# Optimization experiments

Hardware: AMD Instinct MI355X
Metric: run time of the kernel (lower is better)

## Reference

```python
import jax, jax.numpy as jnp
import numpy as np

B, L, D, H, DFF, V, NL = 8, 512, 1024, 16, 4096, 32000, 6
DH = D // H
EPS = 1e-5


def _layer_norm(x):
    # fresh nn.LayerNorm(d_model) each call: gamma=1, beta=0
    mu = jnp.mean(x, axis=-1, keepdims=True)
    var = jnp.var(x, axis=-1, keepdims=True)
    return (x - mu) / jnp.sqrt(var + EPS)


def _positional_encoding(seq_len, d_model, dtype):
    position = jnp.arange(seq_len, dtype=jnp.float32)[:, None]
    div_term = 1.0 / jnp.power(10000.0, jnp.arange(0, d_model, 2, dtype=jnp.float32) / d_model)
    pe = jnp.zeros((seq_len, d_model), dtype=jnp.float32)
    pe = pe.at[:, 0::2].set(jnp.sin(position * div_term))
    pe = pe.at[:, 1::2].set(jnp.cos(position * div_term))
    return pe.astype(dtype)  # [L, D]


def setup_inputs() -> dict:
    key = jax.random.key(0)
    ks = jax.random.split(key, 16)
    s = 0.02
    inp = {
        "sequence": jax.random.randint(ks[0], (B, L), 0, V),
        "segment_label": jax.random.randint(ks[1], (B, L), 0, 3),
        "tok_emb": jax.random.normal(ks[2], (V, D), jnp.float32) * s,
        "seg_emb": jax.random.normal(ks[3], (3, D), jnp.float32) * s,
        "Wq": jax.random.normal(ks[4], (NL, D, D), jnp.float32) * s,
        "bq": jnp.zeros((NL, D), jnp.float32),
        "Wk": jax.random.normal(ks[5], (NL, D, D), jnp.float32) * s,
        "bk": jnp.zeros((NL, D), jnp.float32),
        "Wv": jax.random.normal(ks[6], (NL, D, D), jnp.float32) * s,
        "bv": jnp.zeros((NL, D), jnp.float32),
        "Wo": jax.random.normal(ks[7], (NL, D, D), jnp.float32) * s,
        "bo": jnp.zeros((NL, D), jnp.float32),
        "W1": jax.random.normal(ks[8], (NL, D, DFF), jnp.float32) * s,
        "b1": jnp.zeros((NL, DFF), jnp.float32),
        "W2": jax.random.normal(ks[9], (NL, DFF, D), jnp.float32) * s,
        "b2": jnp.zeros((NL, D), jnp.float32),
    }
    return inp


def reference(sequence, segment_label, tok_emb, seg_emb, Wq, bq, Wk, bk, Wv, bv, Wo, bo, W1, b1, W2, b2):
    n_layers = Wq.shape[0]
    batch, seq_len = sequence.shape
    d_model = tok_emb.shape[1]
    n_heads = H
    dh = d_model // n_heads

    # pad mask: True where key token == 0; broadcast over heads and query positions
    pad = (sequence == 0)  # [B, Lk]
    mask = pad[:, None, None, :]  # [B, 1, 1, Lk]

    pe = _positional_encoding(seq_len, d_model, tok_emb.dtype)
    x = tok_emb[sequence] + pe[None, :, :] + seg_emb[segment_label]  # [B, L, D]

    for i in range(n_layers):
        residual = x
        # NOTE: original code uses a raw reshape [B, L, H*dh] -> [B, H, L, dh]
        # (no transpose); we replicate that exact math.
        q = (x @ Wq[i] + bq[i]).reshape(batch, n_heads, seq_len, dh)
        k = (x @ Wk[i] + bk[i]).reshape(batch, n_heads, seq_len, dh)
        v = (x @ Wv[i] + bv[i]).reshape(batch, n_heads, seq_len, dh)
        scores = jnp.einsum("bhqd,bhkd->bhqk", q, k) / jnp.sqrt(jnp.asarray(dh, x.dtype))
        scores = jnp.where(mask, jnp.asarray(-1e9, x.dtype), scores)
        attn = jax.nn.softmax(scores, axis=-1)
        context = jnp.einsum("bhqk,bhkd->bhqd", attn, v).reshape(batch, seq_len, n_heads * dh)
        out = context @ Wo[i] + bo[i]
        x = _layer_norm(out + residual)

        residual = x
        h = jax.nn.gelu(x @ W1[i] + b1[i], approximate=False)
        out = h @ W2[i] + b2[i]
        x = _layer_norm(residual + out)

    return x
```

## Files before the change

kernel.cpp:

```cpp
#include <hip/hip_runtime.h>
#include <cstdint>
#include <cstddef>

typedef unsigned short u16;
typedef __attribute__((ext_vector_type(8))) short short8;
typedef __attribute__((ext_vector_type(4))) float f32x4;

#define DEV __device__ __forceinline__

DEV float bf2f(u16 u) {
    union { float f; uint32_t i; } c; c.i = ((uint32_t)u) << 16; return c.f;
}
DEV u16 f2bf(float f) {
    union { float f; uint32_t i; } c; c.f = f;
    uint32_t r = c.i + 0x7FFF + ((c.i >> 16) & 1);
    return (u16)(r >> 16);
}

DEV void gload16(const void* g, void* l) {
    __builtin_amdgcn_global_load_lds(
        (const __attribute__((address_space(1))) void*)g,
        (__attribute__((address_space(3))) void*)l, 16, 0, 0);
}

template<int N> DEV void waitv() {
    if constexpr (N == 0)      asm volatile("s_waitcnt vmcnt(0)" ::: "memory");
    else if constexpr (N == 2) asm volatile("s_waitcnt vmcnt(2)" ::: "memory");
    else if constexpr (N == 3) asm volatile("s_waitcnt vmcnt(3)" ::: "memory");
    else if constexpr (N == 4) asm volatile("s_waitcnt vmcnt(4)" ::: "memory");
    else if constexpr (N == 6) asm volatile("s_waitcnt vmcnt(6)" ::: "memory");
    else if constexpr (N == 8) asm volatile("s_waitcnt vmcnt(8)" ::: "memory");
    else                       asm volatile("s_waitcnt vmcnt(0)" ::: "memory");
}

__global__ __launch_bounds__(512)
void attn_kernel(const u16* __restrict__ Qb, const u16* __restrict__ Kb,
                 const u16* __restrict__ vt, const int* __restrict__ seq,
                 u16* __restrict__ ctx)
{
    __shared__ __align__(16) u16 Ss[64 * 512];
    const int tid = threadIdx.x, lane = tid & 63, wid = tid >> 6;
    const int bh = blockIdx.y;
    const int b  = bh >> 4;
    const int q0 = blockIdx.x << 6;
    const u16* Qh = Qb + ((long)bh << 15) + (long)q0 * 64;
    const u16* Kh = Kb + ((long)bh << 15);
    const u16* Vh = vt + ((long)bh << 15);
    const int lr = lane & 15, lk = lane >> 4;

    f32x4 sacc[4][4] = {};
    {
        short8 af[4], bf[4];
#pragma unroll
        for (int s = 0; s < 2; ++s) {
#pragma unroll
            for (int m = 0; m < 4; ++m)
                af[m] = *(const short8*)(Qh + (long)(m * 16 + lr) * 64 + s * 32 + lk * 8);
#pragma unroll
            for (int n = 0; n < 4; ++n)
                bf[n] = *(const short8*)(Kh + (long)(wid * 64 + n * 16 + lr) * 64 + s * 32 + lk * 8);
#pragma unroll
            for (int m = 0; m < 4; ++m)
#pragma unroll
                for (int n = 0; n < 4; ++n)
                    sacc[m][n] = __builtin_amdgcn_mfma_f32_16x16x32_bf16(af[m], bf[n], sacc[m][n], 0, 0, 0);
        }
    }
#pragma unroll
    for (int m = 0; m < 4; ++m) {
#pragma unroll
        for (int n = 0; n < 4; ++n) {
            const int k = wid * 64 + n * 16 + lr;
#pragma unroll
            for (int j = 0; j < 4; ++j) {
                const int q = m * 16 + (lane >> 4) * 4 + j;
                const int col = (((k >> 3) ^ (q & 7)) << 3) | (k & 7);
                Ss[q * 512 + col] = f2bf(sacc[m][n][j] * 0.125f);
            }
        }
    }
    __syncthreads();

    const int* sq = seq + (b << 9) + (lane << 3);
    int msk[8];
#pragma unroll
    for (int i = 0; i < 8; ++i) msk[i] = sq[i];
#pragma unroll
    for (int r = 0; r < 8; ++r) {
        const int q = wid * 8 + r;
        u16* p = Ss + q * 512 + ((lane ^ (q & 7)) << 3);
        short8 raw = *(short8*)p;
        float v[8];
#pragma unroll
        for (int i = 0; i < 8; ++i)
            v[i] = (msk[i] == 0) ? -1e9f : bf2f((u16)raw[i]);
        float mx = v[0];
#pragma unroll
        for (int i = 1; i < 8; ++i) mx = fmaxf(mx, v[i]);
#pragma unroll
        for (int o = 32; o; o >>= 1) mx = fmaxf(mx, __shfl_xor(mx, o));
        float e[8], sum = 0.f;
#pragma unroll
        for (int i = 0; i < 8; ++i) { e[i] = expf(v[i] - mx); sum += e[i]; }
#pragma unroll
        for (int o = 32; o; o >>= 1) sum += __shfl_xor(sum, o);
        float rr = 1.0f / sum;
        short8 o8;
#pragma unroll
        for (int i = 0; i < 8; ++i) o8[i] = (short)f2bf(e[i] * rr);
        *(short8*)p = o8;
    }
    __syncthreads();

    const int wr = wid >> 1, wc2 = wid & 1;
    f32x4 pacc[2] = {};
#pragma unroll
    for (int ks = 0; ks < 16; ++ks) {
        const int qrow = wr * 16 + lr;
        short8 pa = *(const short8*)(Ss + qrow * 512 + (((ks * 4 + lk) ^ (qrow & 7)) << 3));
        short8 vb[2];
#pragma unroll
        for (int n = 0; n < 2; ++n) {
            const int d = wc2 * 32 + n * 16 + lr;
            vb[n] = *(const short8*)(Vh + (long)d * 512 + ks * 32 + lk * 8);
        }
#pragma unroll
        for (int n = 0; n < 2; ++n)
            pacc[n] = __builtin_amdgcn_mfma_f32_16x16x32_bf16(pa, vb[n], pacc[n], 0, 0, 0);
    }
    u16* Ch = ctx + ((long)bh << 15) + (long)q0 * 64;
#pragma unroll
    for (int n = 0; n < 2; ++n) {
        const int d = wc2 * 32 + n * 16 + lr;
#pragma unroll
        for (int j = 0; j < 4; ++j) {
            const int q = wr * 16 + (lane >> 4) * 4 + j;
            Ch[(long)q * 64 + d] = f2bf(pacc[n][j]);
        }
    }
}

template<int EPI>
__global__ __launch_bounds__(512)
void gemm256(const u16* __restrict__ A, const u16* __restrict__ B, void* __restrict__ C,
             const float* __restrict__ bias,
             int K, int lda, int ldb, int ldc)
{
    constexpr int THREADS = 512;
    constexpr int BM = 256, BN = 256, BK = 32;
    constexpr int MR = 8, NR = 4;
    __shared__ __align__(16) u16 As[3 * BM * BK];
    __shared__ __align__(16) u16 Bs[3 * BN * BK];

    const int tid = threadIdx.x, lane = tid & 63, wid = tid >> 6;
    const int wr = wid >> 2, wc = wid & 3;
    const int lr = lane & 15, lk = lane >> 4;
    const int m0 = blockIdx.x * BM, n0 = blockIdx.y * BN;

    f32x4 acc[MR][NR] = {};

    auto stageA = [&](int buf, int k0) {
#pragma unroll
        for (int i = 0; i < 2; ++i) {
            int ch = i * THREADS + tid;
            int rp = ch >> 3, s = ch & 7, d = s ^ (rp & 7);
            const u16* g = A + (long)(m0 + ((rp << 1) | (d & 1))) * lda + k0 + ((d >> 1) << 3);
            gload16(g, (char*)As + (size_t)buf * (BM * BK * 2) + ch * 16);
        }
    };
    auto stageB = [&](int buf, int k0) {
#pragma unroll
        for (int i = 0; i < 2; ++i) {
            int ch = i * THREADS + tid;
            int rp = ch >> 3, s = ch & 7, d = s ^ (rp & 7);
            const u16* g = B + (long)(n0 + ((rp << 1) | (d & 1))) * ldb + k0 + ((d >> 1) << 3);
            gload16(g, (char*)Bs + (size_t)buf * (BN * BK * 2) + ch * 16);
        }
    };
    auto lds_off = [&](int row) -> int {
        int rp = row >> 1;
        int s  = ((lk << 1) | (row & 1)) ^ (rp & 7);
        return rp * 64 + s * 8;
    };

    const int nt = K >> 5;

    stageA(0, 0); stageB(0, 0);
    if (nt > 1) { stageA(1, BK); stageB(1, BK); }
    if (nt > 1) waitv<4>(); else waitv<0>();
    __builtin_amdgcn_s_barrier();

    for (int k = 0; k < nt; ++k) {
        const int cur = k % 3;
        const int nxt = (k + 2) % 3;
        const u16* Ac = As + (size_t)cur * (BM * BK);
        const u16* Bc = Bs + (size_t)cur * (BN * BK);
        short8 af[MR], bf[NR];

#pragma unroll
        for (int n = 0; n < NR; ++n)
            bf[n] = *(const short8*)(Bc + lds_off(wc * 64 + n * 16 + lr));
#pragma unroll
        for (int m = 0; m < 4; ++m)
            af[m] = *(const short8*)(Ac + lds_off(wr * 128 + m * 16 + lr));
        if (k + 2 < nt) stageA(nxt, (k + 2) * BK);
        asm volatile("s_waitcnt lgkmcnt(0)" ::: "memory");
        __builtin_amdgcn_s_setprio(1);
#pragma unroll
        for (int m = 0; m < 4; ++m)
#pragma unroll
            for (int n = 0; n < NR; ++n)
                acc[m][n] = __builtin_amdgcn_mfma_f32_16x16x32_bf16(af[m], bf[n], acc[m][n], 0, 0, 0);
        __builtin_amdgcn_s_setprio(0);

#pragma unroll
        for (int m = 4; m < 8; ++m)
            af[m] = *(const short8*)(Ac + lds_off(wr * 128 + m * 16 + lr));
        if (k + 2 < nt) stageB(nxt, (k + 2) * BK);
        asm volatile("s_waitcnt lgkmcnt(0)" ::: "memory");
        __builtin_amdgcn_s_setprio(1);
#pragma unroll
        for (int m = 4; m < 8; ++m)
#pragma unroll
            for (int n = 0; n < NR; ++n)
                acc[m][n] = __builtin_amdgcn_mfma_f32_16x16x32_bf16(af[m], bf[n], acc[m][n], 0, 0, 0);
        __builtin_amdgcn_s_setprio(0);

        if (k + 1 < nt) {
            if (k + 2 < nt) waitv<4>(); else waitv<0>();
            __builtin_amdgcn_s_barrier();
        }
    }

#pragma unroll
    for (int m = 0; m < MR; ++m) {
        const int rowb = m0 + wr * 128 + m * 16 + (lane >> 4) * 4;
#pragma unroll
        for (int n = 0; n < NR; ++n) {
            const int col = n0 + wc * 64 + n * 16 + lr;
            const float bv = bias[col];
#pragma unroll
            for (int j = 0; j < 4; ++j) {
                float v = acc[m][n][j];
                if (EPI == 2) {
                    float t = v + bv;
                    ((u16*)C)[(long)(rowb + j) * ldc + col] =
                        f2bf(0.5f * t * (1.0f + erff(t * 0.70710678118654752f)));
                } else {
                    const long qidx = (long)(col >> 10) * 4194304L
                                    + (long)(rowb + j) * 1024 + (col & 1023);
                    ((u16*)C)[qidx] = f2bf(v + bv);
                }
            }
        }
    }
}

template<int WM, int WN, int MR, int NR, int EPI>
__global__ __launch_bounds__(WM * WN * 64)
void gemm_bt(const u16* __restrict__ A, const u16* __restrict__ B, void* __restrict__ C,
             const float* __restrict__ bias, const float* __restrict__ resid,
             int K, int lda, int ldb, int ldc,
             int nh, long a_zb, long a_zh, long b_zb, long b_zh, long c_zb, long c_zh,
             float scale)
{
    static_assert(WM * WN == 4 || WM * WN == 8, "4 or 8 waves");
    constexpr int THREADS = WM * WN * 64;
    constexpr int BM = WM * MR * 16;
    constexpr int BN = WN * NR * 16;
    constexpr int BK = 32;
    constexpr int NBUF = 3;
    __shared__ __align__(16) u16 As[NBUF * BM * BK];
    __shared__ __align__(16) u16 Bs[NBUF * BN * BK];

    const int tid  = threadIdx.x;
    const int lane = tid & 63;
    const int wid  = tid >> 6;
    const int zz = blockIdx.z;
    const int b = zz / nh, h = zz % nh;
    A += (long)b * a_zb + (long)h * a_zh;
    B += (long)b * b_zb + (long)h * b_zh;
    const long coff = (long)b * c_zb + (long)h * c_zh;
    const int m0 = blockIdx.x * BM, n0 = blockIdx.y * BN;

    f32x4 acc[MR][NR] = {};
    constexpr int AI = (BM * 4) / THREADS;
    constexpr int BI = (BN * 4) / THREADS;
    constexpr int L  = AI + BI;

    const int wr = wid / WN, wc = wid % WN;
    const int lr = lane & 15, lk = lane >> 4;

    auto stage = [&](int buf, int k0) {
#pragma unroll
        for (int i = 0; i < AI; ++i) {
            int ch = i * THREADS + tid;
            int rp = ch >> 3, s = ch & 7;
            int d  = s ^ (rp & 7);
            const u16* g = A + (long)(m0 + ((rp << 1) | (d & 1))) * lda + k0 + ((d >> 1) << 3);
            gload16(g, (char*)As + (size_t)buf * (BM * BK * 2) + ch * 16);
        }
#pragma unroll
        for (int i = 0; i < BI; ++i) {
            int ch = i * THREADS + tid;
            int rp = ch >> 3, s = ch & 7;
            int d  = s ^ (rp & 7);
            const u16* g = B + (long)(n0 + ((rp << 1) | (d & 1))) * ldb + k0 + ((d >> 1) << 3);
            gload16(g, (char*)Bs + (size_t)buf * (BN * BK * 2) + ch * 16);
        }
    };

    auto lds_off = [&](int row) -> int {
        int rp = row >> 1;
        int s  = ((lk << 1) | (row & 1)) ^ (rp & 7);
        return rp * 64 + s * 8;
    };

    const int nt = K >> 5;

    if (nt > 0) stage(0, 0);
    if (nt > 1) stage(1, BK);
    if (nt > 2) stage(2, 2 * BK);
    if (nt > 2)      waitv<2 * L>();
    else if (nt > 1) waitv<L>();
    else             waitv<0>();
    __builtin_amdgcn_s_barrier();

    for (int k = 0; k < nt; ++k) {
        const int cur = k % 3;
        const u16* Ac = As + (size_t)cur * (BM * BK);
        const u16* Bc = Bs + (size_t)cur * (BN * BK);
        short8 af[MR], bf[NR];
#pragma unroll
        for (int m = 0; m < MR; ++m)
            af[m] = *(const short8*)(Ac + lds_off(wr * MR * 16 + m * 16 + lr));
#pragma unroll
        for (int n = 0; n < NR; ++n)
            bf[n] = *(const short8*)(Bc + lds_off(wc * NR * 16 + n * 16 + lr));

        asm volatile("s_waitcnt lgkmcnt(0)" ::: "memory");
        __builtin_amdgcn_s_barrier();

        if (k + 3 < nt) stage(cur, (k + 3) * BK);

#pragma unroll
        for (int m = 0; m < MR; ++m)
#pragma unroll
            for (int n = 0; n < NR; ++n)
                acc[m][n] = __builtin_amdgcn_mfma_f32_16x16x32_bf16(af[m], bf[n], acc[m][n], 0, 0, 0);

        if (k + 1 < nt) {
            if (k + 4 <= nt)      waitv<2 * L>();
            else if (k + 3 == nt) waitv<L>();
            else                  waitv<0>();
            __builtin_amdgcn_s_barrier();
        }
    }

#pragma unroll
    for (int m = 0; m < MR; ++m) {
        const int rowb = m0 + wr * MR * 16 + m * 16 + (lane >> 4) * 4;
#pragma unroll
        for (int n = 0; n < NR; ++n) {
            const int col = n0 + wc * NR * 16 + n * 16 + lr;
            float bv = 0.f;
            if (EPI == 0 || EPI == 1 || EPI == 2 || EPI == 5) bv = bias[col];
#pragma unroll
            for (int j = 0; j < 4; ++j) {
                const long idx = coff + (long)(rowb + j) * ldc + col;
                float v = acc[m][n][j];
                if (EPI == 0) {
                    ((u16*)C)[idx] = f2bf(v + bv);
                } else if (EPI == 1) {
                    ((float*)C)[idx] = v + bv + resid[(long)(rowb + j) * ldc + col];
                } else if (EPI == 2) {
                    float t = v + bv;
                    ((u16*)C)[idx] = f2bf(0.5f * t * (1.0f + erff(t * 0.70710678118654752f)));
                } else if (EPI == 3) {
                    ((u16*)C)[idx] = f2bf(v * scale);
                } else if (EPI == 5) {
                    const long qidx = (long)(col >> 10) * 4194304L
                                    + (long)(rowb + j) * 1024 + (col & 1023);
                    ((u16*)C)[qidx] = f2bf(v + bv);
                } else {
                    ((u16*)C)[idx] = f2bf(v);
                }
            }
        }
    }
}

__global__ __launch_bounds__(256)
void wconv_kernel(const float* __restrict__ src, u16* __restrict__ dst,
                  int K, int N, int row_off)
{
    __shared__ __align__(16) float t[64][65];
    const float* s = src + (long)(blockIdx.y * 64) * N + blockIdx.x * 64;
    const int tid = threadIdx.x;
#pragma unroll
    for (int i = 0; i < 4; ++i) {
        int ch = (i << 8) + tid;
        int r = ch >> 4, c4 = ch & 15;
        float4 v = *(const float4*)(s + (long)r * N + c4 * 4);
        t[r][c4 * 4 + 0] = v.x; t[r][c4 * 4 + 1] = v.y;
        t[r][c4 * 4 + 2] = v.z; t[r][c4 * 4 + 3] = v.w;
    }
    __syncthreads();
    u16* d = dst + (long)(row_off + blockIdx.x * 64) * K + blockIdx.y * 64;
#pragma unroll
    for (int i = 0; i < 4; ++i) {
        int ch = (i << 8) + tid;
        int c = ch >> 4, k4 = ch & 15;
        ushort4 o;
        o.x = f2bf(t[k4 * 4 + 0][c]);
        o.y = f2bf(t[k4 * 4 + 1][c]);
        o.z = f2bf(t[k4 * 4 + 2][c]);
        o.w = f2bf(t[k4 * 4 + 3][c]);
        *(ushort4*)(d + (long)c * K + k4 * 4) = o;
    }
}

__global__ __launch_bounds__(256)
void bconcat_kernel(const float* __restrict__ bq, const float* __restrict__ bk,
                    const float* __restrict__ bv, float* __restrict__ out)
{
    int i = blockIdx.x * 256 + threadIdx.x;
    int l = i / 3072, n = i % 3072;
    float v = (n < 1024) ? bq[l * 1024 + n]
            : (n < 2048) ? bk[l * 1024 + n - 1024]
                         : bv[l * 1024 + n - 2048];
    out[i] = v;
}

__global__ __launch_bounds__(256)
void embed_kernel(const int* __restrict__ seq, const int* __restrict__ seg,
                  const float* __restrict__ tok, const float* __restrict__ sege,
                  float* __restrict__ x, u16* __restrict__ xb)
{
    long i = ((long)blockIdx.x << 8) + threadIdx.x;
    int d2 = (int)(i & 511);
    long bl = i >> 9;
    int l = (int)(bl & 511);
    int t = seq[bl];
    int g = seg[bl];
    float div = powf(10000.f, -(float)(2 * d2) * (1.0f / 1024.f));
    float arg = (float)l * div;
    float sv = sinf(arg), cv = cosf(arg);
    long toff = (long)t * 1024 + 2 * d2;
    long goff = (long)g * 1024 + 2 * d2;
    float x0 = tok[toff]     + sv + sege[goff];
    float x1 = tok[toff + 1] + cv + sege[goff + 1];
    long xo = (bl << 10) + 2 * d2;
    x[xo] = x0; x[xo + 1] = x1;
    xb[xo] = f2bf(x0); xb[xo + 1] = f2bf(x1);
}

__global__ __launch_bounds__(256)
void vtrans_kernel(const u16* __restrict__ Vb, u16* __restrict__ vt)
{
    __shared__ __align__(16) u16 t[64][72];
    const int bh = blockIdx.y;
    const int l0 = blockIdx.x << 6;
    const u16* src = Vb + ((long)bh << 15) + (long)l0 * 64;
    const int tid = threadIdx.x;
#pragma unroll
    for (int i = 0; i < 2; ++i) {
        int ch = (i << 8) + tid;
        int r = ch >> 3, c8 = ch & 7;
        short8 v = *(const short8*)(src + (long)r * 64 + (c8 << 3));
#pragma unroll
        for (int j = 0; j < 8; ++j) t[r][(c8 << 3) + j] = (u16)v[j];
    }
    __syncthreads();
    u16* d = vt + ((long)bh << 15) + l0;
#pragma unroll
    for (int i = 0; i < 2; ++i) {
        int ch = (i << 8) + tid;
        int dd = ch >> 3, l8 = ch & 7;
        short8 o;
#pragma unroll
        for (int j = 0; j < 8; ++j) o[j] = (short)t[(l8 << 3) + j][dd];
        *(short8*)(d + (long)dd * 512 + (l8 << 3)) = o;
    }
}

__global__ __launch_bounds__(256)
void ln_kernel(const float* __restrict__ in, float* __restrict__ xout, u16* __restrict__ xbout)
{
    const int row = blockIdx.x;
    const int tid = threadIdx.x;
    const float4 v = ((const float4*)(in + (long)row * 1024))[tid];
    float s = v.x + v.y + v.z + v.w;
#pragma unroll
    for (int o = 32; o; o >>= 1) s += __shfl_down(s, o);
    __shared__ float red[8];
    const int wid = tid >> 6, lane = tid & 63;
    if (lane == 0) red[wid] = s;
    __syncthreads();
    const float mean = (red[0] + red[1] + red[2] + red[3]) * (1.0f / 1024.f);
    const float dx = v.x - mean, dy = v.y - mean, dz = v.z - mean, dw = v.w - mean;
    float q = dx * dx + dy * dy + dz * dz + dw * dw;
#pragma unroll
    for (int o = 32; o; o >>= 1) q += __shfl_down(q, o);
    if (lane == 0) red[4 + wid] = q;
    __syncthreads();
    const float var = (red[4] + red[5] + red[6] + red[7]) * (1.0f / 1024.f);
    const float inv = rsqrtf(var + 1e-5f);
    float4 o4;
    o4.x = dx * inv; o4.y = dy * inv; o4.z = dz * inv; o4.w = dw * inv;
    ((float4*)(xout + (long)row * 1024))[tid] = o4;
    ushort4 ob;
    ob.x = f2bf(o4.x); ob.y = f2bf(o4.y); ob.z = f2bf(o4.z); ob.w = f2bf(o4.w);
    ((ushort4*)(xbout + (long)row * 1024))[tid] = ob;
}

extern "C" void kernel_launch(void* const* d_in, const int* in_sizes, int n_in,
                              void* d_out, int out_size, void* d_ws, size_t ws_size,
                              hipStream_t stream)
{
    const int*   seqp = (const int*)d_in[0];
    const int*   segp = (const int*)d_in[1];
    const float* tok  = (const float*)d_in[2];
    const float* sege = (const float*)d_in[3];
    const float* Wq = (const float*)d_in[4];  const float* bq = (const float*)d_in[5];
    const float* Wk = (const float*)d_in[6];  const float* bk = (const float*)d_in[7];
    const float* Wv = (const float*)d_in[8];  const float* bv = (const float*)d_in[9];
    const float* Wo = (const float*)d_in[10]; const float* bo = (const float*)d_in[11];
    const float* W1 = (const float*)d_in[12]; const float* b1 = (const float*)d_in[13];
    const float* W2 = (const float*)d_in[14]; const float* b2 = (const float*)d_in[15];

    char* w = (char*)d_ws;
    auto take = [&](size_t bytes) -> void* {
        void* p = (void*)w; w += (bytes + 255) & ~(size_t)255; return p;
    };
    float* x    = (float*)take(4096UL * 1024 * 4);
    u16*   xb   = (u16*)  take(4096UL * 1024 * 2);
    float* tmp  = (float*)take(4096UL * 1024 * 4);
    u16*   R1   = (u16*)  take(128UL * 512 * 512 * 2);
    u16*   qkv3 = (u16*)  take(3UL * 4096 * 1024 * 2);
    u16*   ctx  = (u16*)  take(4096UL * 1024 * 2);
    u16*   vt   = (u16*)  take(128UL * 64 * 512 * 2);
    u16*   qkvw = (u16*)  take(3072UL * 1024 * 2);
    u16*   wo_t = (u16*)  take(1024UL * 1024 * 2);
    u16*   w1_t = (u16*)  take(4096UL * 1024 * 2);
    u16*   w2_t = (u16*)  take(1024UL * 4096 * 2);
    float* bqkv = (float*)take(6UL * 3072 * 4);

    u16* hbuf = R1;
    u16* Qb   = qkv3;
    u16* Kb   = qkv3 + 4194304L;
    u16* Vb   = qkv3 + 8388608L;

    bconcat_kernel<<<72, 256, 0, stream>>>(bq, bk, bv, bqkv);
    embed_kernel<<<8192, 256, 0, stream>>>(seqp, segp, tok, sege, x, xb);

    for (int l = 0; l < 6; ++l) {
        wconv_kernel<<<dim3(16, 16), 256, 0, stream>>>(Wq + (long)l * 1048576L, qkvw, 1024, 1024, 0);
        wconv_kernel<<<dim3(16, 16), 256, 0, stream>>>(Wk + (long)l * 1048576L, qkvw, 1024, 1024, 1024);
        wconv_kernel<<<dim3(16, 16), 256, 0, stream>>>(Wv + (long)l * 1048576L, qkvw, 1024, 1024, 2048);
        wconv_kernel<<<dim3(16, 16), 256, 0, stream>>>(Wo + (long)l * 1048576L, wo_t, 1024, 1024, 0);
        wconv_kernel<<<dim3(64, 16), 256, 0, stream>>>(W1 + (long)l * 4194304L, w1_t, 1024, 4096, 0);
        wconv_kernel<<<dim3(16, 64), 256, 0, stream>>>(W2 + (long)l * 4194304L, w2_t, 4096, 1024, 0);

        gemm256<5><<<dim3(16, 12), 512, 0, stream>>>(
            xb, qkvw, qkv3, bqkv + l * 3072, 1024, 1024, 1024, 1024);

        vtrans_kernel<<<dim3(8, 128), 256, 0, stream>>>(Vb, vt);

        attn_kernel<<<dim3(8, 128), 512, 0, stream>>>(Qb, Kb, vt, seqp, ctx);

        gemm_bt<2, 4, 4, 2, 1><<<dim3(32, 8, 1), 512, 0, stream>>>(
            ctx, wo_t, tmp, bo + l * 1024, x,
            1024, 1024, 1024, 1024, 1, 0, 0, 0, 0, 0, 0, 1.f);

        ln_kernel<<<4096, 256, 0, stream>>>(tmp, x, xb);

        gemm256<2><<<dim3(16, 16), 512, 0, stream>>>(
            xb, w1_t, hbuf, b1 + l * 4096, 1024, 1024, 1024, 4096);

        gemm_bt<2, 4, 4, 2, 1><<<dim3(32, 8, 1), 512, 0, stream>>>(
            hbuf, w2_t, tmp, b2 + l * 1024, x,
            4096, 4096, 4096, 1024, 1, 0, 0, 0, 0, 0, 0, 1.f);

        ln_kernel<<<4096, 256, 0, stream>>>(tmp, (l == 5) ? (float*)d_out : x, xb);
    }
}
```

Measured before the change: 1.744 ms.

## Use K-blocked 64-wide activation/weight layout with unified 128x128 BK=64 GEMM

All GEMM operands (activations, context, FFN hidden, converted weights) are now stored in a K-blocked layout of 64-column planes. This lets a single new gemm_k64 kernel (128x128 tiles, BK=64, 3-stage buffering) load contiguous 128-byte rows per plane, and it replaces both gemm256 and gemm_bt. Weight conversion for all six layers is hoisted out of the layer loop into six batched launches, and the producers (embed, LN, attention epilogue, GELU epilogue) write directly into the blocked layout. The cost is a larger workspace for the full set of converted weights, smaller tiles for the QKV and FFN1 GEMMs, and scattered epilogue stores.

Result: slower. 1.899 ms (+8.9%).

```diff
diff --git a/kernel.cpp b/kernel.cpp
--- a/kernel.cpp
+++ b/kernel.cpp
@@ -25,18 +25,132 @@
 
 template<int N> DEV void waitv() {
     if constexpr (N == 0)      asm volatile("s_waitcnt vmcnt(0)" ::: "memory");
-    else if constexpr (N == 2) asm volatile("s_waitcnt vmcnt(2)" ::: "memory");
-    else if constexpr (N == 3) asm volatile("s_waitcnt vmcnt(3)" ::: "memory");
     else if constexpr (N == 4) asm volatile("s_waitcnt vmcnt(4)" ::: "memory");
-    else if constexpr (N == 6) asm volatile("s_waitcnt vmcnt(6)" ::: "memory");
     else if constexpr (N == 8) asm volatile("s_waitcnt vmcnt(8)" ::: "memory");
     else                       asm volatile("s_waitcnt vmcnt(0)" ::: "memory");
+}
+
+template<int EPI>
+__global__ __launch_bounds__(512)
+void gemm_k64(const u16* __restrict__ Ablk, const u16* __restrict__ Bblk,
+              void* __restrict__ C, const float* __restrict__ bias,
+              const float* __restrict__ resid, int K, int Mtot, int Ntot)
+{
+    constexpr int THREADS = 512;
+    constexpr int BM = 128, BN = 128;
+    constexpr int MR = 4, NR = 2;
+    __shared__ __align__(16) u16 As[3 * BM * 64];
+    __shared__ __align__(16) u16 Bs[3 * BN * 64];
+
+    const int tid = threadIdx.x, lane = tid & 63, wid = tid >> 6;
+    const int wr = wid >> 2, wc = wid & 3;
+    const int lr = lane & 15, lk = lane >> 4;
+    const int m0 = blockIdx.x * BM, n0 = blockIdx.y * BN;
+    const long planeA = (long)Mtot * 64, planeB = (long)Ntot * 64;
+
+    f32x4 acc[MR][NR] = {};
+
+    auto stageA = [&](int buf, int k0) {
+#pragma unroll
+        for (int i = 0; i < 2; ++i) {
+            int ch = i * THREADS + tid;
+            int row = ch >> 3, s = ch & 7, d = s ^ (row & 7);
+            const u16* g = Ablk + (long)(k0 >> 6) * planeA + (long)(m0 + row) * 64 + d * 8;
+            gload16(g, (char*)As + (size_t)buf * (BM * 128) + ch * 16);
+        }
+    };
+    auto stageB = [&](int buf, int k0) {
+#pragma unroll
+        for (int i = 0; i < 2; ++i) {
+            int ch = i * THREADS + tid;
+            int row = ch >> 3, s = ch & 7, d = s ^ (row & 7);
+            const u16* g = Bblk + (long)(k0 >> 6) * planeB + (long)(n0 + row) * 64 + d * 8;
+            gload16(g, (char*)Bs + (size_t)buf * (BN * 128) + ch * 16);
+        }
+    };
+    auto lds_off = [&](int row, int ks) -> int {
+        return row * 64 + ((ks ^ (row & 7)) << 3);
+    };
+
+    const int nt = K >> 6;
+
+    stageA(0, 0); stageB(0, 0);
+    if (nt > 1) { stageA(1, 64); stageB(1, 64); }
+    if (nt > 2) { stageA(2, 128); stageB(2, 128); }
+    if (nt > 2)      waitv<8>();
+    else if (nt > 1) waitv<4>();
+    else             waitv<0>();
+    __builtin_amdgcn_s_barrier();
+
+    for (int k = 0; k < nt; ++k) {
+        const int cur = k % 3;
+        const u16* Ac = As + (size_t)cur * (BM * 64);
+        const u16* Bc = Bs + (size_t)cur * (BN * 64);
+        short8 af[2][MR], bf[2][NR];
+#pragma unroll
+        for (int h = 0; h < 2; ++h) {
+#pragma unroll
+            for (int m = 0; m < MR; ++m)
+                af[h][m] = *(const short8*)(Ac + lds_off(wr * 64 + m * 16 + lr, h * 4 + lk));
+#pragma unroll
+            for (int n = 0; n < NR; ++n)
+                bf[h][n] = *(const short8*)(Bc + lds_off(wc * 32 + n * 16 + lr, h * 4 + lk));
+        }
+
+        asm volatile("s_waitcnt lgkmcnt(0)" ::: "memory");
+        __builtin_amdgcn_s_barrier();
+
+        if (k + 3 < nt) { stageA(cur, (k + 3) * 64); stageB(cur, (k + 3) * 64); }
+
+        __builtin_amdgcn_s_setprio(1);
+#pragma unroll
+        for (int h = 0; h < 2; ++h)
+#pragma unroll
+            for (int m = 0; m < MR; ++m)
+#pragma unroll
+                for (int n = 0; n < NR; ++n)
+                    acc[m][n] = __builtin_amdgcn_mfma_f32_16x16x32_bf16(af[h][m], bf[h][n], acc[m][n], 0, 0, 0);
+        __builtin_amdgcn_s_setprio(0);
+
+        if (k + 1 < nt) {
+            if (k + 4 <= nt)      waitv<8>();
+            else if (k + 3 == nt) waitv<4>();
+            else                  waitv<0>();
+            __builtin_amdgcn_s_barrier();
+        }
+    }
+
+#pragma unroll
+    for (int m = 0; m < MR; ++m) {
+        const int rowb = m0 + wr * 64 + m * 16 + (lane >> 4) * 4;
+#pragma unroll
+        for (int n = 0; n < NR; ++n) {
+            const int col = n0 + wc * 32 + n * 16 + lr;
+            const float bv = bias[col];
+#pragma unroll
+            for (int j = 0; j < 4; ++j) {
+                float v = acc[m][n][j];
+                if (EPI == 1) {
+                    const long idx = (long)(rowb + j) * 1024 + col;
+                    ((float*)C)[idx] = v + bv + resid[idx];
+                } else if (EPI == 5) {
+                    const long qidx = (long)(col >> 10) * 4194304L
+                                    + (long)(rowb + j) * 1024 + (col & 1023);
+                    ((u16*)C)[qidx] = f2bf(v + bv);
+                } else {
+                    float t = v + bv;
+                    ((u16*)C)[(long)(col >> 6) * 262144L + (long)(rowb + j) * 64 + (col & 63)]
+                        = f2bf(0.5f * t * (1.0f + erff(t * 0.70710678118654752f)));
+                }
+            }
+        }
+    }
 }
 
 __global__ __launch_bounds__(512)
 void attn_kernel(const u16* __restrict__ Qb, const u16* __restrict__ Kb,
                  const u16* __restrict__ vt, const int* __restrict__ seq,
-                 u16* __restrict__ ctx)
+                 u16* __restrict__ ctxB)
 {
     __shared__ __align__(16) u16 Ss[64 * 512];
     const int tid = threadIdx.x, lane = tid & 63, wid = tid >> 6;
@@ -128,274 +242,28 @@
         for (int n = 0; n < 2; ++n)
             pacc[n] = __builtin_amdgcn_mfma_f32_16x16x32_bf16(pa, vb[n], pacc[n], 0, 0, 0);
     }
-    u16* Ch = ctx + ((long)bh << 15) + (long)q0 * 64;
 #pragma unroll
     for (int n = 0; n < 2; ++n) {
         const int d = wc2 * 32 + n * 16 + lr;
 #pragma unroll
         for (int j = 0; j < 4; ++j) {
             const int q = wr * 16 + (lane >> 4) * 4 + j;
-            Ch[(long)q * 64 + d] = f2bf(pacc[n][j]);
-        }
-    }
-}
-
-template<int EPI>
-__global__ __launch_bounds__(512)
-void gemm256(const u16* __restrict__ A, const u16* __restrict__ B, void* __restrict__ C,
-             const float* __restrict__ bias,
-             int K, int lda, int ldb, int ldc)
-{
-    constexpr int THREADS = 512;
-    constexpr int BM = 256, BN = 256, BK = 32;
-    constexpr int MR = 8, NR = 4;
-    __shared__ __align__(16) u16 As[3 * BM * BK];
-    __shared__ __align__(16) u16 Bs[3 * BN * BK];
-
-    const int tid = threadIdx.x, lane = tid & 63, wid = tid >> 6;
-    const int wr = wid >> 2, wc = wid & 3;
-    const int lr = lane & 15, lk = lane >> 4;
-    const int m0 = blockIdx.x * BM, n0 = blockIdx.y * BN;
-
-    f32x4 acc[MR][NR] = {};
-
-    auto stageA = [&](int buf, int k0) {
-#pragma unroll
-        for (int i = 0; i < 2; ++i) {
-            int ch = i * THREADS + tid;
-            int rp = ch >> 3, s = ch & 7, d = s ^ (rp & 7);
-            const u16* g = A + (long)(m0 + ((rp << 1) | (d & 1))) * lda + k0 + ((d >> 1) << 3);
-            gload16(g, (char*)As + (size_t)buf * (BM * BK * 2) + ch * 16);
-        }
-    };
-    auto stageB = [&](int buf, int k0) {
-#pragma unroll
-        for (int i = 0; i < 2; ++i) {
-            int ch = i * THREADS + tid;
-            int rp = ch >> 3, s = ch & 7, d = s ^ (rp & 7);
-            const u16* g = B + (long)(n0 + ((rp << 1) | (d & 1))) * ldb + k0 + ((d >> 1) << 3);
-            gload16(g, (char*)Bs + (size_t)buf * (BN * BK * 2) + ch * 16);
-        }
-    };
-    auto lds_off = [&](int row) -> int {
-        int rp = row >> 1;
-        int s  = ((lk << 1) | (row & 1)) ^ (rp & 7);
-        return rp * 64 + s * 8;
-    };
-
-    const int nt = K >> 5;
-
-    stageA(0, 0); stageB(0, 0);
-    if (nt > 1) { stageA(1, BK); stageB(1, BK); }
-    if (nt > 1) waitv<4>(); else waitv<0>();
-    __builtin_amdgcn_s_barrier();
-
-    for (int k = 0; k < nt; ++k) {
-        const int cur = k % 3;
-        const int nxt = (k + 2) % 3;
-        const u16* Ac = As + (size_t)cur * (BM * BK);
-        const u16* Bc = Bs + (size_t)cur * (BN * BK);
-        short8 af[MR], bf[NR];
-
-#pragma unroll
-        for (int n = 0; n < NR; ++n)
-            bf[n] = *(const short8*)(Bc + lds_off(wc * 64 + n * 16 + lr));
-#pragma unroll
-        for (int m = 0; m < 4; ++m)
-            af[m] = *(const short8*)(Ac + lds_off(wr * 128 + m * 16 + lr));
-        if (k + 2 < nt) stageA(nxt, (k + 2) * BK);
-        asm volatile("s_waitcnt lgkmcnt(0)" ::: "memory");
-        __builtin_amdgcn_s_setprio(1);
-#pragma unroll
-        for (int m = 0; m < 4; ++m)
-#pragma unroll
-            for (int n = 0; n < NR; ++n)
-                acc[m][n] = __builtin_amdgcn_mfma_f32_16x16x32_bf16(af[m], bf[n], acc[m][n], 0, 0, 0);
-        __builtin_amdgcn_s_setprio(0);
-
-#pragma unroll
-        for (int m = 4; m < 8; ++m)
-            af[m] = *(const short8*)(Ac + lds_off(wr * 128 + m * 16 + lr));
-        if (k + 2 < nt) stageB(nxt, (k + 2) * BK);
-        asm volatile("s_waitcnt lgkmcnt(0)" ::: "memory");
-        __builtin_amdgcn_s_setprio(1);
-#pragma unroll
-        for (int m = 4; m < 8; ++m)
-#pragma unroll
-            for (int n = 0; n < NR; ++n)
-                acc[m][n] = __builtin_amdgcn_mfma_f32_16x16x32_bf16(af[m], bf[n], acc[m][n], 0, 0, 0);
-        __builtin_amdgcn_s_setprio(0);
-
-        if (k + 1 < nt) {
-            if (k + 2 < nt) waitv<4>(); else waitv<0>();
-            __builtin_amdgcn_s_barrier();
-        }
-    }
-
-#pragma unroll
-    for (int m = 0; m < MR; ++m) {
-        const int rowb = m0 + wr * 128 + m * 16 + (lane >> 4) * 4;
-#pragma unroll
-        for (int n = 0; n < NR; ++n) {
-            const int col = n0 + wc * 64 + n * 16 + lr;
-            const float bv = bias[col];
-#pragma unroll
-            for (int j = 0; j < 4; ++j) {
-                float v = acc[m][n][j];
-                if (EPI == 2) {
-                    float t = v + bv;
-                    ((u16*)C)[(long)(rowb + j) * ldc + col] =
-                        f2bf(0.5f * t * (1.0f + erff(t * 0.70710678118654752f)));
-                } else {
-                    const long qidx = (long)(col >> 10) * 4194304L
-                                    + (long)(rowb + j) * 1024 + (col & 1023);
-                    ((u16*)C)[qidx] = f2bf(v + bv);
-                }
-            }
-        }
-    }
-}
-
-template<int WM, int WN, int MR, int NR, int EPI>
-__global__ __launch_bounds__(WM * WN * 64)
-void gemm_bt(const u16* __restrict__ A, const u16* __restrict__ B, void* __restrict__ C,
-             const float* __restrict__ bias, const float* __restrict__ resid,
-             int K, int lda, int ldb, int ldc,
-             int nh, long a_zb, long a_zh, long b_zb, long b_zh, long c_zb, long c_zh,
-             float scale)
-{
-    static_assert(WM * WN == 4 || WM * WN == 8, "4 or 8 waves");
-    constexpr int THREADS = WM * WN * 64;
-    constexpr int BM = WM * MR * 16;
-    constexpr int BN = WN * NR * 16;
-    constexpr int BK = 32;
-    constexpr int NBUF = 3;
-    __shared__ __align__(16) u16 As[NBUF * BM * BK];
-    __shared__ __align__(16) u16 Bs[NBUF * BN * BK];
-
-    const int tid  = threadIdx.x;
-    const int lane = tid & 63;
-    const int wid  = tid >> 6;
-    const int zz = blockIdx.z;
-    const int b = zz / nh, h = zz % nh;
-    A += (long)b * a_zb + (long)h * a_zh;
-    B += (long)b * b_zb + (long)h * b_zh;
-    const long coff = (long)b * c_zb + (long)h * c_zh;
-    const int m0 = blockIdx.x * BM, n0 = blockIdx.y * BN;
-
-    f32x4 acc[MR][NR] = {};
-    constexpr int AI = (BM * 4) / THREADS;
-    constexpr int BI = (BN * 4) / THREADS;
-    constexpr int L  = AI + BI;
-
-    const int wr = wid / WN, wc = wid % WN;
-    const int lr = lane & 15, lk = lane >> 4;
-
-    auto stage = [&](int buf, int k0) {
-#pragma unroll
-        for (int i = 0; i < AI; ++i) {
-            int ch = i * THREADS + tid;
-            int rp = ch >> 3, s = ch & 7;
-            int d  = s ^ (rp & 7);
-            const u16* g = A + (long)(m0 + ((rp << 1) | (d & 1))) * lda + k0 + ((d >> 1) << 3);
-            gload16(g, (char*)As + (size_t)buf * (BM * BK * 2) + ch * 16);
-        }
-#pragma unroll
-        for (int i = 0; i < BI; ++i) {
-            int ch = i * THREADS + tid;
-            int rp = ch >> 3, s = ch & 7;
-            int d  = s ^ (rp & 7);
-            const u16* g = B + (long)(n0 + ((rp << 1) | (d & 1))) * ldb + k0 + ((d >> 1) << 3);
-            gload16(g, (char*)Bs + (size_t)buf * (BN * BK * 2) + ch * 16);
-        }
-    };
-
-    auto lds_off = [&](int row) -> int {
-        int rp = row >> 1;
-        int s  = ((lk << 1) | (row & 1)) ^ (rp & 7);
-        return rp * 64 + s * 8;
-    };
-
-    const int nt = K >> 5;
-
-    if (nt > 0) stage(0, 0);
-    if (nt > 1) stage(1, BK);
-    if (nt > 2) stage(2, 2 * BK);
-    if (nt > 2)      waitv<2 * L>();
-    else if (nt > 1) waitv<L>();
-    else             waitv<0>();
-    __builtin_amdgcn_s_barrier();
-
-    for (int k = 0; k < nt; ++k) {
-        const int cur = k % 3;
-        const u16* Ac = As + (size_t)cur * (BM * BK);
-        const u16* Bc = Bs + (size_t)cur * (BN * BK);
-        short8 af[MR], bf[NR];
-#pragma unroll
-        for (int m = 0; m < MR; ++m)
-            af[m] = *(const short8*)(Ac + lds_off(wr * MR * 16 + m * 16 + lr));
-#pragma unroll
-        for (int n = 0; n < NR; ++n)
-            bf[n] = *(const short8*)(Bc + lds_off(wc * NR * 16 + n * 16 + lr));
-
-        asm volatile("s_waitcnt lgkmcnt(0)" ::: "memory");
-        __builtin_amdgcn_s_barrier();
-
-        if (k + 3 < nt) stage(cur, (k + 3) * BK);
-
-#pragma unroll
-        for (int m = 0; m < MR; ++m)
-#pragma unroll
-            for (int n = 0; n < NR; ++n)
-                acc[m][n] = __builtin_amdgcn_mfma_f32_16x16x32_bf16(af[m], bf[n], acc[m][n], 0, 0, 0);
-
-        if (k + 1 < nt) {
-            if (k + 4 <= nt)      waitv<2 * L>();
-            else if (k + 3 == nt) waitv<L>();
-            else                  waitv<0>();
-            __builtin_amdgcn_s_barrier();
-        }
-    }
-
-#pragma unroll
-    for (int m = 0; m < MR; ++m) {
-        const int rowb = m0 + wr * MR * 16 + m * 16 + (lane >> 4) * 4;
-#pragma unroll
-        for (int n = 0; n < NR; ++n) {
-            const int col = n0 + wc * NR * 16 + n * 16 + lr;
-            float bv = 0.f;
-            if (EPI == 0 || EPI == 1 || EPI == 2 || EPI == 5) bv = bias[col];
-#pragma unroll
-            for (int j = 0; j < 4; ++j) {
-                const long idx = coff + (long)(rowb + j) * ldc + col;
-                float v = acc[m][n][j];
-                if (EPI == 0) {
-                    ((u16*)C)[idx] = f2bf(v + bv);
-                } else if (EPI == 1) {
-                    ((float*)C)[idx] = v + bv + resid[(long)(rowb + j) * ldc + col];
-                } else if (EPI == 2) {
-                    float t = v + bv;
-                    ((u16*)C)[idx] = f2bf(0.5f * t * (1.0f + erff(t * 0.70710678118654752f)));
-                } else if (EPI == 3) {
-                    ((u16*)C)[idx] = f2bf(v * scale);
-                } else if (EPI == 5) {
-                    const long qidx = (long)(col >> 10) * 4194304L
-                                    + (long)(rowb + j) * 1024 + (col & 1023);
-                    ((u16*)C)[qidx] = f2bf(v + bv);
-                } else {
-                    ((u16*)C)[idx] = f2bf(v);
-                }
-            }
+            const long F = ((long)bh << 15) + (long)(q0 + q) * 64 + d;
+            const long r = F >> 10;
+            const int  c = (int)(F & 1023);
+            ctxB[(long)(c >> 6) * 262144L + r * 64 + (c & 63)] = f2bf(pacc[n][j]);
         }
     }
 }
 
 __global__ __launch_bounds__(256)
-void wconv_kernel(const float* __restrict__ src, u16* __restrict__ dst,
-                  int K, int N, int row_off)
+void wconv_blk(const float* __restrict__ src, u16* __restrict__ dst,
+               int N, int planeN, int row_off, long src_z, long dst_z)
 {
     __shared__ __align__(16) float t[64][65];
-    const float* s = src + (long)(blockIdx.y * 64) * N + blockIdx.x * 64;
+    const int z = blockIdx.z;
+    const int k0 = blockIdx.x * 64, n0 = blockIdx.y * 64;
+    const float* s = src + (long)z * src_z + (long)k0 * N + n0;
     const int tid = threadIdx.x;
 #pragma unroll
     for (int i = 0; i < 4; ++i) {
@@ -406,7 +274,7 @@
         t[r][c4 * 4 + 2] = v.z; t[r][c4 * 4 + 3] = v.w;
     }
     __syncthreads();
-    u16* d = dst + (long)(row_off + blockIdx.x * 64) * K + blockIdx.y * 64;
+    u16* d = dst + (long)z * dst_z + (long)blockIdx.x * planeN * 64 + (long)(row_off + n0) * 64;
 #pragma unroll
     for (int i = 0; i < 4; ++i) {
         int ch = (i << 8) + tid;
@@ -416,7 +284,7 @@
         o.y = f2bf(t[k4 * 4 + 1][c]);
         o.z = f2bf(t[k4 * 4 + 2][c]);
         o.w = f2bf(t[k4 * 4 + 3][c]);
-        *(ushort4*)(d + (long)c * K + k4 * 4) = o;
+        *(ushort4*)(d + (long)c * 64 + k4 * 4) = o;
     }
 }
 
@@ -435,7 +303,7 @@
 __global__ __launch_bounds__(256)
 void embed_kernel(const int* __restrict__ seq, const int* __restrict__ seg,
                   const float* __restrict__ tok, const float* __restrict__ sege,
-                  float* __restrict__ x, u16* __restrict__ xb)
+                  float* __restrict__ x, u16* __restrict__ xbB)
 {
     long i = ((long)blockIdx.x << 8) + threadIdx.x;
     int d2 = (int)(i & 511);
@@ -452,7 +320,9 @@
     float x1 = tok[toff + 1] + cv + sege[goff + 1];
     long xo = (bl << 10) + 2 * d2;
     x[xo] = x0; x[xo + 1] = x1;
-    xb[xo] = f2bf(x0); xb[xo + 1] = f2bf(x1);
+    const int c = 2 * d2;
+    u16* p = xbB + (long)(c >> 6) * 262144L + bl * 64 + (c & 63);
+    p[0] = f2bf(x0); p[1] = f2bf(x1);
 }
 
 __global__ __launch_bounds__(256)
@@ -485,7 +355,7 @@
 }
 
 __global__ __launch_bounds__(256)
-void ln_kernel(const float* __restrict__ in, float* __restrict__ xout, u16* __restrict__ xbout)
+void ln_kernel(const float* __restrict__ in, float* __restrict__ xout, u16* __restrict__ xbB)
 {
     const int row = blockIdx.x;
     const int tid = threadIdx.x;
@@ -511,7 +381,7 @@
     ((float4*)(xout + (long)row * 1024))[tid] = o4;
     ushort4 ob;
     ob.x = f2bf(o4.x); ob.y = f2bf(o4.y); ob.z = f2bf(o4.z); ob.w = f2bf(o4.w);
-    ((ushort4*)(xbout + (long)row * 1024))[tid] = ob;
+    *(ushort4*)(xbB + (long)(tid >> 4) * 262144L + (long)row * 64 + (tid & 15) * 4) = ob;
 }
 
 extern "C" void kernel_launch(void* const* d_in, const int* in_sizes, int n_in,
@@ -534,54 +404,55 @@
         void* p = (void*)w; w += (bytes + 255) & ~(size_t)255; return p;
     };
     float* x    = (float*)take(4096UL * 1024 * 4);
-    u16*   xb   = (u16*)  take(4096UL * 1024 * 2);
+    u16*   xbB  = (u16*)  take(4096UL * 1024 * 2);
     float* tmp  = (float*)take(4096UL * 1024 * 4);
-    u16*   R1   = (u16*)  take(128UL * 512 * 512 * 2);
+    u16*   hbuf = (u16*)  take(4096UL * 4096 * 2);
     u16*   qkv3 = (u16*)  take(3UL * 4096 * 1024 * 2);
-    u16*   ctx  = (u16*)  take(4096UL * 1024 * 2);
+    u16*   ctxB = (u16*)  take(4096UL * 1024 * 2);
     u16*   vt   = (u16*)  take(128UL * 64 * 512 * 2);
-    u16*   qkvw = (u16*)  take(3072UL * 1024 * 2);
-    u16*   wo_t = (u16*)  take(1024UL * 1024 * 2);
-    u16*   w1_t = (u16*)  take(4096UL * 1024 * 2);
-    u16*   w2_t = (u16*)  take(1024UL * 4096 * 2);
+    u16*   qkvwB= (u16*)  take(6UL * 3072 * 1024 * 2);
+    u16*   woB  = (u16*)  take(6UL * 1024 * 1024 * 2);
+    u16*   w1B  = (u16*)  take(6UL * 4096 * 1024 * 2);
+    u16*   w2B  = (u16*)  take(6UL * 1024 * 4096 * 2);
     float* bqkv = (float*)take(6UL * 3072 * 4);
 
-    u16* hbuf = R1;
-    u16* Qb   = qkv3;
-    u16* Kb   = qkv3 + 4194304L;
-    u16* Vb   = qkv3 + 8388608L;
+    u16* Qb = qkv3;
+    u16* Kb = qkv3 + 4194304L;
+    u16* Vb = qkv3 + 8388608L;
 
     bconcat_kernel<<<72, 256, 0, stream>>>(bq, bk, bv, bqkv);
-    embed_kernel<<<8192, 256, 0, stream>>>(seqp, segp, tok, sege, x, xb);
+    wconv_blk<<<dim3(16, 16, 6), 256, 0, stream>>>(Wq, qkvwB, 1024, 3072, 0,    1048576L, 3145728L);
+    wconv_blk<<<dim3(16, 16, 6), 256, 0, stream>>>(Wk, qkvwB, 1024, 3072, 1024, 1048576L, 3145728L);
+    wconv_blk<<<dim3(16, 16, 6), 256, 0, stream>>>(Wv, qkvwB, 1024, 3072, 2048, 1048576L, 3145728L);
+    wconv_blk<<<dim3(16, 16, 6), 256, 0, stream>>>(Wo, woB,   1024, 1024, 0,    1048576L, 1048576L);
+    wconv_blk<<<dim3(16, 64, 6), 256, 0, stream>>>(W1, w1B,   4096, 4096, 0,    4194304L, 4194304L);
+    wconv_blk<<<dim3(64, 16, 6), 256, 0, stream>>>(W2, w2B,   1024, 1024, 0,    4194304L, 4194304L);
+
+    embed_kernel<<<8192, 256, 0, stream>>>(seqp, segp, tok, sege, x, xbB);
 
     for (int l = 0; l < 6; ++l) {
-        wconv_kernel<<<dim3(16, 16), 256, 0, stream>>>(Wq + (long)l * 1048576L, qkvw, 1024, 1024, 0);
-        wconv_kernel<<<dim3(16, 16), 256, 0, stream>>>(Wk + (long)l * 1048576L, qkvw, 1024, 1024, 1024);
-        wconv_kernel<<<dim3(16, 16), 256, 0, stream>>>(Wv + (long)l * 1048576L, qkvw, 1024, 1024, 2048);
-        wconv_kernel<<<dim3(16, 16), 256, 0, stream>>>(Wo + (long)l * 1048576L, wo_t, 1024, 1024, 0);
-        wconv_kernel<<<dim3(64, 16), 256, 0, stream>>>(W1 + (long)l * 4194304L, w1_t, 1024, 4096, 0);
-        wconv_kernel<<<dim3(16, 64), 256, 0, stream>>>(W2 + (long)l * 4194304L, w2_t, 4096, 1024, 0);
-
-        gemm256<5><<<dim3(16, 12), 512, 0, stream>>>(
-            xb, qkvw, qkv3, bqkv + l * 3072, 1024, 1024, 1024, 1024);
+        gemm_k64<5><<<dim3(32, 24), 512, 0, stream>>>(
+            xbB, qkvwB + (long)l * 3145728L, qkv3, bqkv + l * 3072, nullptr,
+            1024, 4096, 3072);
 
         vtrans_kernel<<<dim3(8, 128), 256, 0, stream>>>(Vb, vt);
 
-        attn_kernel<<<dim3(8, 128), 512, 0, stream>>>(Qb, Kb, vt, seqp, ctx);
-
-        gemm_bt<2, 4, 4, 2, 1><<<dim3(32, 8, 1), 512, 0, stream>>>(
-            ctx, wo_t, tmp, bo + l * 1024, x,
-            1024, 1024, 1024, 1024, 1, 0, 0, 0, 0, 0, 0, 1.f);
-
-        ln_kernel<<<4096, 256, 0, stream>>>(tmp, x, xb);
-
-        gemm256<2><<<dim3(16, 16), 512, 0, stream>>>(
-            xb, w1_t, hbuf, b1 + l * 4096, 1024, 1024, 1024, 4096);
-
-        gemm_bt<2, 4, 4, 2, 1><<<dim3(32, 8, 1), 512, 0, stream>>>(
-            hbuf, w2_t, tmp, b2 + l * 1024, x,
-            4096, 4096, 4096, 1024, 1, 0, 0, 0, 0, 0, 0, 1.f);
-
-        ln_kernel<<<4096, 256, 0, stream>>>(tmp, (l == 5) ? (float*)d_out : x, xb);
-    }
-}
+        attn_kernel<<<dim3(8, 128), 512, 0, stream>>>(Qb, Kb, vt, seqp, ctxB);
+
+        gemm_k64<1><<<dim3(32, 8), 512, 0, stream>>>(
+            ctxB, woB + (long)l * 1048576L, tmp, bo + l * 1024, x,
+            1024, 4096, 1024);
+
+        ln_kernel<<<4096, 256, 0, stream>>>(tmp, x, xbB);
+
+        gemm_k64<6><<<dim3(32, 32), 512, 0, stream>>>(
+            xbB, w1B + (long)l * 4194304L, hbuf, b1 + l * 4096, nullptr,
+            1024, 4096, 4096);
+
+        gemm_k64<1><<<dim3(32, 8), 512, 0, stream>>>(
+            hbuf, w2B + (long)l * 4194304L, tmp, b2 + l * 1024, x,
+            4096, 4096, 1024);
+
+        ln_kernel<<<4096, 256, 0, stream>>>(tmp, (l == 5) ? (float*)d_out : x, xbB);
+    }
+}
```
